# Performance work log

Measured on AMD Instinct MI355X. Metric: run time of the kernel, lower is better.

Reference implementation:

```python
import jax, jax.numpy as jnp
import numpy as np

B, S, H, E, K = 4, 4096, 2048, 64, 8
SEQ_ALPHA = 0.01


def setup_inputs() -> dict:
    key = jax.random.key(0)
    k1, k2 = jax.random.split(key)
    x = jax.random.normal(k1, (B, S, H), dtype=jnp.float32)
    # kaiming_uniform_(a=sqrt(5)) on [E, H] -> bound = 1/sqrt(H)
    bound = 1.0 / np.sqrt(H)
    weight = jax.random.uniform(k2, (E, H), dtype=jnp.float32, minval=-bound, maxval=bound)
    expert_bias = jnp.zeros((E,), dtype=jnp.float32)
    return {"x": x, "weight": weight, "expert_bias": expert_bias}


def reference(x, weight, expert_bias):
    bsz, seq_len, _ = x.shape
    x_flat = x.reshape(-1, x.shape[-1])                      # [T, H], T = B*S
    logits = x_flat @ weight.T                               # [T, E]
    scores = jax.nn.sigmoid(logits)
    biased_logits = logits + expert_bias[None, :]
    _, topk_idx = jax.lax.top_k(biased_logits, K)            # [T, K] int32
    topk_w = jnp.take_along_axis(scores, topk_idx, axis=-1)  # [T, K]
    topk_w = topk_w / (topk_w.sum(axis=-1, keepdims=True) + 1e-10)  # K > 1
    # load stats (training-mode bincount)
    expert_load = jnp.bincount(topk_idx.reshape(-1), length=E).astype(jnp.int64)
    # sequence-wise balance loss (DeepSeek-V3)
    scores_r = scores.reshape(bsz, seq_len, E)
    expert_mask = jax.nn.one_hot(topk_idx.reshape(bsz, -1), E, dtype=scores.dtype)  # [B, S*K, E]
    f_i = expert_mask.sum(axis=1) / (K * seq_len)            # [B, E]
    normalized = scores_r / (scores_r.sum(axis=2, keepdims=True) + 1e-10)
    P_i = normalized.mean(axis=1)                            # [B, E]
    aux_seq_loss = SEQ_ALPHA * (f_i * P_i).sum(axis=1).mean()
    return (topk_idx, topk_w, aux_seq_loss, expert_load)
```

## Files before the change

kernel.cpp:

```cpp
#include <hip/hip_runtime.h>
#include <math.h>

#define HDIM 2048
#define TTOK 16384
#define NEXP 64
#define TOPK 8
#define SLEN 4096
#define NBATCH 4

#define OFF_W    131072
#define OFF_LOSS 262144
#define OFF_LOAD 262145

#define WS_PACC 0
#define WS_CACC 256
#define WS_CNT  512
#define WS_WH   1024
#define WS_WL   (1024 + 65536)

using s16x8 = __attribute__((ext_vector_type(8))) short;
using f32x4 = __attribute__((ext_vector_type(4))) float;

__device__ __forceinline__ unsigned bfh(float v) {
  unsigned b = __float_as_uint(v);
  return (b + 0x7FFFu + ((b >> 16) & 1u)) >> 16;
}

__device__ __forceinline__ void split4(float4 v, uint2* hi, uint2* lo) {
  unsigned h0 = bfh(v.x), h1 = bfh(v.y), h2 = bfh(v.z), h3 = bfh(v.w);
  float r0 = v.x - __uint_as_float(h0 << 16);
  float r1 = v.y - __uint_as_float(h1 << 16);
  float r2 = v.z - __uint_as_float(h2 << 16);
  float r3 = v.w - __uint_as_float(h3 << 16);
  unsigned l0 = bfh(r0), l1 = bfh(r1), l2 = bfh(r2), l3 = bfh(r3);
  *hi = make_uint2(h0 | (h1 << 16), h2 | (h3 << 16));
  *lo = make_uint2(l0 | (l1 << 16), l2 | (l3 << 16));
}

__global__ __launch_bounds__(256) void prep_w(const float* __restrict__ W,
                                              ushort* __restrict__ Wh,
                                              ushort* __restrict__ Wl) {
  const int i = (blockIdx.x * 256 + threadIdx.x) << 2;
  float4 v = *(const float4*)(W + i);
  uint2 hp, lp;
  split4(v, &hp, &lp);
  *(uint2*)(Wh + i) = hp;
  *(uint2*)(Wl + i) = lp;
}

__global__ __launch_bounds__(1024) void gate_fused(
    const float* __restrict__ x,
    const ushort* __restrict__ Whg,
    const ushort* __restrict__ Wlg,
    const float* __restrict__ bias,
    float* __restrict__ out, float* __restrict__ Pacc,
    float* __restrict__ Cacc, int* __restrict__ counter) {
  __shared__ ushort XhL[2][4096];
  __shared__ ushort XlL[2][4096];
  __shared__ ushort WhL[2][4096];
  __shared__ ushort WlL[2][4096];
  __shared__ float le[64 * 65];
  __shared__ float sgm[64 * 65];
  __shared__ float rinvs[64];
  __shared__ float biasl[64];
  __shared__ unsigned csum[64];
  __shared__ int lastf;

  const int tid = threadIdx.x;
  const int lane = tid & 63;
  const int wv = __builtin_amdgcn_readfirstlane(tid >> 6);
  const int tok0 = blockIdx.x << 6;

  if (tid < 64) { csum[tid] = 0u; biasl[tid] = bias[tid]; }

  const int srow = tid >> 4;
  const int skq = (tid & 15) << 2;
  const int sdst = (srow << 6) + (((skq >> 3) ^ (srow & 7)) << 3) +
                   (((skq >> 2) & 1) << 2);
  const float* xsrc = x + (size_t)(tok0 + srow) * HDIM + skq;
  const ushort* whsrc = Whg + ((size_t)srow << 11) + skq;
  const ushort* wlsrc = Wlg + ((size_t)srow << 11) + skq;

  float4 xA = *(const float4*)xsrc;
  float4 xB = *(const float4*)(xsrc + 64);
  uint2 whA = *(const uint2*)whsrc;
  uint2 whB = *(const uint2*)(whsrc + 64);
  uint2 wlA = *(const uint2*)wlsrc;
  uint2 wlB = *(const uint2*)(wlsrc + 64);

  const int mt = wv >> 2, nt = wv & 3;
  const int fl = lane & 15, fg = lane >> 4;
  const int arow = (mt << 4) + fl;
  const int brow = (nt << 4) + fl;
  const int ab0 = (arow << 6) + ((fg ^ (arow & 7)) << 3);
  const int ab1 = (arow << 6) + (((fg + 4) ^ (arow & 7)) << 3);
  const int bb0 = (brow << 6) + ((fg ^ (brow & 7)) << 3);
  const int bb1 = (brow << 6) + (((fg + 4) ^ (brow & 7)) << 3);

  f32x4 acc = {0.f, 0.f, 0.f, 0.f};

  constexpr int NT = HDIM / 64;
  for (int kt = 0; kt < NT; ++kt) {
    const int cur = kt & 1;
    {
      uint2 hp, lp;
      split4(xA, &hp, &lp);
      *(uint2*)&XhL[cur][sdst] = hp;
      *(uint2*)&XlL[cur][sdst] = lp;
      *(uint2*)&WhL[cur][sdst] = whA;
      *(uint2*)&WlL[cur][sdst] = wlA;
    }
    __syncthreads();
    xA = xB; whA = whB; wlA = wlB;
    if (kt + 2 < NT) {
      xB = *(const float4*)(xsrc + ((kt + 2) << 6));
      whB = *(const uint2*)(whsrc + ((kt + 2) << 6));
      wlB = *(const uint2*)(wlsrc + ((kt + 2) << 6));
    }
    s16x8 ah0 = *(const s16x8*)&XhL[cur][ab0];
    s16x8 al0 = *(const s16x8*)&XlL[cur][ab0];
    s16x8 bh0 = *(const s16x8*)&WhL[cur][bb0];
    s16x8 bl0 = *(const s16x8*)&WlL[cur][bb0];
    acc = __builtin_amdgcn_mfma_f32_16x16x32_bf16(al0, bh0, acc, 0, 0, 0);
    acc = __builtin_amdgcn_mfma_f32_16x16x32_bf16(ah0, bl0, acc, 0, 0, 0);
    acc = __builtin_amdgcn_mfma_f32_16x16x32_bf16(ah0, bh0, acc, 0, 0, 0);
    s16x8 ah1 = *(const s16x8*)&XhL[cur][ab1];
    s16x8 al1 = *(const s16x8*)&XlL[cur][ab1];
    s16x8 bh1 = *(const s16x8*)&WhL[cur][bb1];
    s16x8 bl1 = *(const s16x8*)&WlL[cur][bb1];
    acc = __builtin_amdgcn_mfma_f32_16x16x32_bf16(al1, bh1, acc, 0, 0, 0);
    acc = __builtin_amdgcn_mfma_f32_16x16x32_bf16(ah1, bl1, acc, 0, 0, 0);
    acc = __builtin_amdgcn_mfma_f32_16x16x32_bf16(ah1, bh1, acc, 0, 0, 0);
  }

  {
    const int trow = (mt << 4) + (fg << 2);
    const int ecol = (nt << 4) + fl;
#pragma unroll
    for (int r = 0; r < 4; ++r) {
      float lg = acc[r];
      le[(trow + r) * 65 + ecol] = lg;
      sgm[(trow + r) * 65 + ecol] = 1.f / (1.f + expf(-lg));
    }
  }
  __syncthreads();

  const int b = (int)(blockIdx.x >> 6);

  if (wv == 0) {
    const int t = lane;
    float bl[64];
#pragma unroll
    for (int e = 0; e < NEXP; ++e) bl[e] = le[t * 65 + e] + biasl[e];

    unsigned long long chosen = 0ull;
    int i8[TOPK];
    float w8[TOPK];
    float wsum = 0.f;
#pragma unroll
    for (int j = 0; j < TOPK; ++j) {
      float best = -1e30f;
      int bi = 0;
#pragma unroll
      for (int e = 0; e < NEXP; ++e) {
        bool ok = (((chosen >> e) & 1ull) == 0ull) && (bl[e] > best);
        if (ok) { best = bl[e]; bi = e; }
      }
      chosen |= (1ull << bi);
      float sc = sgm[t * 65 + bi];
      i8[j] = bi;
      w8[j] = sc;
      wsum += sc;
    }
    const float inv = 1.f / (wsum + 1e-10f);
    const int tt = tok0 + t;
    float4 o;
    o.x = (float)i8[0]; o.y = (float)i8[1]; o.z = (float)i8[2]; o.w = (float)i8[3];
    *(float4*)(out + (size_t)tt * TOPK) = o;
    o.x = (float)i8[4]; o.y = (float)i8[5]; o.z = (float)i8[6]; o.w = (float)i8[7];
    *(float4*)(out + (size_t)tt * TOPK + 4) = o;
    o.x = w8[0] * inv; o.y = w8[1] * inv; o.z = w8[2] * inv; o.w = w8[3] * inv;
    *(float4*)(out + OFF_W + (size_t)tt * TOPK) = o;
    o.x = w8[4] * inv; o.y = w8[5] * inv; o.z = w8[6] * inv; o.w = w8[7] * inv;
    *(float4*)(out + OFF_W + (size_t)tt * TOPK + 4) = o;
#pragma unroll
    for (int j = 0; j < TOPK; ++j) atomicAdd(&csum[i8[j]], 1u);
    atomicAdd(&Cacc[(b << 6) + lane], (float)csum[lane]);
  } else if (wv == 1) {
    const int t = lane;
    float ss = 0.f;
    for (int e = 0; e < NEXP; ++e) ss += sgm[t * 65 + e];
    rinvs[t] = 1.f / (ss + 1e-10f);
    float p = 0.f;
    for (int t2 = 0; t2 < 64; ++t2) p += sgm[t2 * 65 + lane] * rinvs[t2];
    atomicAdd(&Pacc[(b << 6) + lane], p);
  }

  __syncthreads();
  __threadfence();
  if (tid == 0) {
    int old = __hip_atomic_fetch_add(counter, 1, __ATOMIC_ACQ_REL,
                                     __HIP_MEMORY_SCOPE_AGENT);
    lastf = (old == 255) ? 1 : 0;
  }
  __syncthreads();

  if (lastf && tid < 64) {
    const int e = tid;
    float load = 0.f, partl = 0.f;
#pragma unroll
    for (int bb = 0; bb < NBATCH; ++bb) {
      float c = __hip_atomic_load(&Cacc[(bb << 6) + e], __ATOMIC_RELAXED,
                                  __HIP_MEMORY_SCOPE_AGENT);
      float p = __hip_atomic_load(&Pacc[(bb << 6) + e], __ATOMIC_RELAXED,
                                  __HIP_MEMORY_SCOPE_AGENT);
      load += c;
      partl += (c * (1.f / (TOPK * (float)SLEN))) * (p * (1.f / (float)SLEN));
    }
    out[OFF_LOAD + e] = load;
#pragma unroll
    for (int off = 32; off; off >>= 1) partl += __shfl_down(partl, off);
    if (e == 0) out[OFF_LOSS] = 0.01f * partl * (1.f / (float)NBATCH);
  }
}

extern "C" void kernel_launch(void* const* d_in, const int* in_sizes, int n_in,
                              void* d_out, int out_size, void* d_ws, size_t ws_size,
                              hipStream_t stream) {
  const float* x = (const float*)d_in[0];
  const float* W = (const float*)d_in[1];
  const float* bias = (const float*)d_in[2];
  float* out = (float*)d_out;

  float* ws = (float*)d_ws;
  float* Pacc = ws + WS_PACC;
  float* Cacc = ws + WS_CACC;
  int* counter = (int*)(ws + WS_CNT);
  ushort* Wh = (ushort*)(ws + WS_WH);
  ushort* Wl = (ushort*)(ws + WS_WL);

  hipMemsetAsync(ws, 0, 1024 * sizeof(float), stream);
  prep_w<<<128, 256, 0, stream>>>(W, Wh, Wl);
  gate_fused<<<256, 1024, 0, stream>>>(x, Wh, Wl, bias, out, Pacc, Cacc, counter);
}
```

Baseline: 287.0 us.

## Use 16-token tiles with weights pre-swizzled into MFMA fragment layout read from global

Repacks the split bf16 weight into a per-lane MFMA fragment layout so each wave loads its B operands straight from global/L2 instead of staging them through LDS. Blocks shrink from 64 tokens and 1024 threads to 16 tokens and 256 threads, giving 1024 blocks and much less shared memory per block so more blocks fit per CU. The trade-off is that the weight is re-read from cache by four times as many blocks, and the top-k stage now uses only 16 lanes of one wave.

```diff
diff --git a/kernel.cpp b/kernel.cpp
--- a/kernel.cpp
+++ b/kernel.cpp
@@ -15,8 +15,9 @@
 #define WS_PACC 0
 #define WS_CACC 256
 #define WS_CNT  512
-#define WS_WH   1024
-#define WS_WL   (1024 + 65536)
+#define WS_WF   1024
+#define WFLO    131072
+#define NBLK    1024
 
 using s16x8 = __attribute__((ext_vector_type(8))) short;
 using f32x4 = __attribute__((ext_vector_type(4))) float;
@@ -37,39 +38,50 @@
   *lo = make_uint2(l0 | (l1 << 16), l2 | (l3 << 16));
 }
 
-__global__ __launch_bounds__(256) void prep_w(const float* __restrict__ W,
-                                              ushort* __restrict__ Wh,
-                                              ushort* __restrict__ Wl) {
-  const int i = (blockIdx.x * 256 + threadIdx.x) << 2;
-  float4 v = *(const float4*)(W + i);
-  uint2 hp, lp;
-  split4(v, &hp, &lp);
-  *(uint2*)(Wh + i) = hp;
-  *(uint2*)(Wl + i) = lp;
-}
-
-__global__ __launch_bounds__(1024) void gate_fused(
+__global__ __launch_bounds__(256) void prep_wf(const float* __restrict__ W,
+                                               ushort* __restrict__ WF) {
+  const int id = blockIdx.x * 256 + threadIdx.x;
+  const int lane = id & 63;
+  const int reg = (id >> 6) & 1;
+  const int nt = (id >> 7) & 3;
+  const int kt = (id >> 9) & 31;
+  const int plane = id >> 14;
+  const int e = (nt << 4) + (lane & 15);
+  const int k0 = (kt << 6) + (reg << 5) + ((lane >> 4) << 3);
+  const float* src = W + (size_t)e * HDIM + k0;
+  unsigned w[4];
+#pragma unroll
+  for (int j = 0; j < 4; ++j) {
+    float v0 = src[2 * j], v1 = src[2 * j + 1];
+    unsigned h0 = bfh(v0), h1 = bfh(v1);
+    if (plane) {
+      h0 = bfh(v0 - __uint_as_float(h0 << 16));
+      h1 = bfh(v1 - __uint_as_float(h1 << 16));
+    }
+    w[j] = h0 | (h1 << 16);
+  }
+  *(uint4*)(WF + ((size_t)id << 3)) = make_uint4(w[0], w[1], w[2], w[3]);
+}
+
+__global__ __launch_bounds__(256, 8) void gate_fused(
     const float* __restrict__ x,
-    const ushort* __restrict__ Whg,
-    const ushort* __restrict__ Wlg,
+    const ushort* __restrict__ WF,
     const float* __restrict__ bias,
     float* __restrict__ out, float* __restrict__ Pacc,
     float* __restrict__ Cacc, int* __restrict__ counter) {
-  __shared__ ushort XhL[2][4096];
-  __shared__ ushort XlL[2][4096];
-  __shared__ ushort WhL[2][4096];
-  __shared__ ushort WlL[2][4096];
-  __shared__ float le[64 * 65];
-  __shared__ float sgm[64 * 65];
-  __shared__ float rinvs[64];
+  __shared__ ushort XhL[2][1024];
+  __shared__ ushort XlL[2][1024];
+  __shared__ float le[16 * 65];
+  __shared__ float sgm[16 * 65];
+  __shared__ float rinvs[16];
   __shared__ float biasl[64];
   __shared__ unsigned csum[64];
   __shared__ int lastf;
 
   const int tid = threadIdx.x;
   const int lane = tid & 63;
-  const int wv = __builtin_amdgcn_readfirstlane(tid >> 6);
-  const int tok0 = blockIdx.x << 6;
+  const int nt = __builtin_amdgcn_readfirstlane(tid >> 6);
+  const int tok0 = blockIdx.x << 4;
 
   if (tid < 64) { csum[tid] = 0u; biasl[tid] = bias[tid]; }
 
@@ -78,24 +90,14 @@
   const int sdst = (srow << 6) + (((skq >> 3) ^ (srow & 7)) << 3) +
                    (((skq >> 2) & 1) << 2);
   const float* xsrc = x + (size_t)(tok0 + srow) * HDIM + skq;
-  const ushort* whsrc = Whg + ((size_t)srow << 11) + skq;
-  const ushort* wlsrc = Wlg + ((size_t)srow << 11) + skq;
-
   float4 xA = *(const float4*)xsrc;
   float4 xB = *(const float4*)(xsrc + 64);
-  uint2 whA = *(const uint2*)whsrc;
-  uint2 whB = *(const uint2*)(whsrc + 64);
-  uint2 wlA = *(const uint2*)wlsrc;
-  uint2 wlB = *(const uint2*)(wlsrc + 64);
-
-  const int mt = wv >> 2, nt = wv & 3;
+
   const int fl = lane & 15, fg = lane >> 4;
-  const int arow = (mt << 4) + fl;
-  const int brow = (nt << 4) + fl;
+  const int arow = fl;
   const int ab0 = (arow << 6) + ((fg ^ (arow & 7)) << 3);
   const int ab1 = (arow << 6) + (((fg + 4) ^ (arow & 7)) << 3);
-  const int bb0 = (brow << 6) + ((fg ^ (brow & 7)) << 3);
-  const int bb1 = (brow << 6) + (((fg + 4) ^ (brow & 7)) << 3);
+  const ushort* wbase = WF + ((size_t)((nt << 7) + lane) << 3);
 
   f32x4 acc = {0.f, 0.f, 0.f, 0.f};
 
@@ -107,34 +109,29 @@
       split4(xA, &hp, &lp);
       *(uint2*)&XhL[cur][sdst] = hp;
       *(uint2*)&XlL[cur][sdst] = lp;
-      *(uint2*)&WhL[cur][sdst] = whA;
-      *(uint2*)&WlL[cur][sdst] = wlA;
     }
     __syncthreads();
-    xA = xB; whA = whB; wlA = wlB;
-    if (kt + 2 < NT) {
-      xB = *(const float4*)(xsrc + ((kt + 2) << 6));
-      whB = *(const uint2*)(whsrc + ((kt + 2) << 6));
-      wlB = *(const uint2*)(wlsrc + ((kt + 2) << 6));
-    }
+    xA = xB;
+    if (kt + 2 < NT) xB = *(const float4*)(xsrc + ((kt + 2) << 6));
+    const ushort* whp = wbase + (kt << 12);
+    s16x8 bh0 = *(const s16x8*)whp;
+    s16x8 bh1 = *(const s16x8*)(whp + 512);
+    s16x8 bl0 = *(const s16x8*)(whp + WFLO);
+    s16x8 bl1 = *(const s16x8*)(whp + WFLO + 512);
     s16x8 ah0 = *(const s16x8*)&XhL[cur][ab0];
     s16x8 al0 = *(const s16x8*)&XlL[cur][ab0];
-    s16x8 bh0 = *(const s16x8*)&WhL[cur][bb0];
-    s16x8 bl0 = *(const s16x8*)&WlL[cur][bb0];
+    s16x8 ah1 = *(const s16x8*)&XhL[cur][ab1];
+    s16x8 al1 = *(const s16x8*)&XlL[cur][ab1];
     acc = __builtin_amdgcn_mfma_f32_16x16x32_bf16(al0, bh0, acc, 0, 0, 0);
     acc = __builtin_amdgcn_mfma_f32_16x16x32_bf16(ah0, bl0, acc, 0, 0, 0);
     acc = __builtin_amdgcn_mfma_f32_16x16x32_bf16(ah0, bh0, acc, 0, 0, 0);
-    s16x8 ah1 = *(const s16x8*)&XhL[cur][ab1];
-    s16x8 al1 = *(const s16x8*)&XlL[cur][ab1];
-    s16x8 bh1 = *(const s16x8*)&WhL[cur][bb1];
-    s16x8 bl1 = *(const s16x8*)&WlL[cur][bb1];
     acc = __builtin_amdgcn_mfma_f32_16x16x32_bf16(al1, bh1, acc, 0, 0, 0);
     acc = __builtin_amdgcn_mfma_f32_16x16x32_bf16(ah1, bl1, acc, 0, 0, 0);
     acc = __builtin_amdgcn_mfma_f32_16x16x32_bf16(ah1, bh1, acc, 0, 0, 0);
   }
 
   {
-    const int trow = (mt << 4) + (fg << 2);
+    const int trow = fg << 2;
     const int ecol = (nt << 4) + fl;
 #pragma unroll
     for (int r = 0; r < 4; ++r) {
@@ -145,54 +142,59 @@
   }
   __syncthreads();
 
-  const int b = (int)(blockIdx.x >> 6);
-
-  if (wv == 0) {
-    const int t = lane;
-    float bl[64];
-#pragma unroll
-    for (int e = 0; e < NEXP; ++e) bl[e] = le[t * 65 + e] + biasl[e];
-
-    unsigned long long chosen = 0ull;
-    int i8[TOPK];
-    float w8[TOPK];
-    float wsum = 0.f;
-#pragma unroll
-    for (int j = 0; j < TOPK; ++j) {
-      float best = -1e30f;
-      int bi = 0;
-#pragma unroll
-      for (int e = 0; e < NEXP; ++e) {
-        bool ok = (((chosen >> e) & 1ull) == 0ull) && (bl[e] > best);
-        if (ok) { best = bl[e]; bi = e; }
+  const int b = (int)(blockIdx.x >> 8);
+
+  if (nt == 0) {
+    if (lane < 16) {
+      const int t = lane;
+      float bl[64];
+#pragma unroll
+      for (int e = 0; e < NEXP; ++e) bl[e] = le[t * 65 + e] + biasl[e];
+
+      unsigned long long chosen = 0ull;
+      int i8[TOPK];
+      float w8[TOPK];
+      float wsum = 0.f;
+#pragma unroll
+      for (int j = 0; j < TOPK; ++j) {
+        float best = -1e30f;
+        int bi = 0;
+#pragma unroll
+        for (int e = 0; e < NEXP; ++e) {
+          bool ok = (((chosen >> e) & 1ull) == 0ull) && (bl[e] > best);
+          if (ok) { best = bl[e]; bi = e; }
+        }
+        chosen |= (1ull << bi);
+        float sc = sgm[t * 65 + bi];
+        i8[j] = bi;
+        w8[j] = sc;
+        wsum += sc;
       }
-      chosen |= (1ull << bi);
-      float sc = sgm[t * 65 + bi];
-      i8[j] = bi;
-      w8[j] = sc;
-      wsum += sc;
-    }
-    const float inv = 1.f / (wsum + 1e-10f);
-    const int tt = tok0 + t;
-    float4 o;
-    o.x = (float)i8[0]; o.y = (float)i8[1]; o.z = (float)i8[2]; o.w = (float)i8[3];
-    *(float4*)(out + (size_t)tt * TOPK) = o;
-    o.x = (float)i8[4]; o.y = (float)i8[5]; o.z = (float)i8[6]; o.w = (float)i8[7];
-    *(float4*)(out + (size_t)tt * TOPK + 4) = o;
-    o.x = w8[0] * inv; o.y = w8[1] * inv; o.z = w8[2] * inv; o.w = w8[3] * inv;
-    *(float4*)(out + OFF_W + (size_t)tt * TOPK) = o;
-    o.x = w8[4] * inv; o.y = w8[5] * inv; o.z = w8[6] * inv; o.w = w8[7] * inv;
-    *(float4*)(out + OFF_W + (size_t)tt * TOPK + 4) = o;
-#pragma unroll
-    for (int j = 0; j < TOPK; ++j) atomicAdd(&csum[i8[j]], 1u);
+      const float inv = 1.f / (wsum + 1e-10f);
+      const int tt = tok0 + t;
+      float4 o;
+      o.x = (float)i8[0]; o.y = (float)i8[1]; o.z = (float)i8[2]; o.w = (float)i8[3];
+      *(float4*)(out + (size_t)tt * TOPK) = o;
+      o.x = (float)i8[4]; o.y = (float)i8[5]; o.z = (float)i8[6]; o.w = (float)i8[7];
+      *(float4*)(out + (size_t)tt * TOPK + 4) = o;
+      o.x = w8[0] * inv; o.y = w8[1] * inv; o.z = w8[2] * inv; o.w = w8[3] * inv;
+      *(float4*)(out + OFF_W + (size_t)tt * TOPK) = o;
+      o.x = w8[4] * inv; o.y = w8[5] * inv; o.z = w8[6] * inv; o.w = w8[7] * inv;
+      *(float4*)(out + OFF_W + (size_t)tt * TOPK + 4) = o;
+#pragma unroll
+      for (int j = 0; j < TOPK; ++j) atomicAdd(&csum[i8[j]], 1u);
+    }
     atomicAdd(&Cacc[(b << 6) + lane], (float)csum[lane]);
-  } else if (wv == 1) {
-    const int t = lane;
-    float ss = 0.f;
-    for (int e = 0; e < NEXP; ++e) ss += sgm[t * 65 + e];
-    rinvs[t] = 1.f / (ss + 1e-10f);
+  } else if (nt == 1) {
+    if (lane < 16) {
+      const int t = lane;
+      float ss = 0.f;
+      for (int e = 0; e < NEXP; ++e) ss += sgm[t * 65 + e];
+      rinvs[t] = 1.f / (ss + 1e-10f);
+    }
     float p = 0.f;
-    for (int t2 = 0; t2 < 64; ++t2) p += sgm[t2 * 65 + lane] * rinvs[t2];
+#pragma unroll
+    for (int t2 = 0; t2 < 16; ++t2) p += sgm[t2 * 65 + lane] * rinvs[t2];
     atomicAdd(&Pacc[(b << 6) + lane], p);
   }
 
@@ -201,7 +203,7 @@
   if (tid == 0) {
     int old = __hip_atomic_fetch_add(counter, 1, __ATOMIC_ACQ_REL,
                                      __HIP_MEMORY_SCOPE_AGENT);
-    lastf = (old == 255) ? 1 : 0;
+    lastf = (old == NBLK - 1) ? 1 : 0;
   }
   __syncthreads();
 
@@ -236,10 +238,9 @@
   float* Pacc = ws + WS_PACC;
   float* Cacc = ws + WS_CACC;
   int* counter = (int*)(ws + WS_CNT);
-  ushort* Wh = (ushort*)(ws + WS_WH);
-  ushort* Wl = (ushort*)(ws + WS_WL);
+  ushort* WF = (ushort*)(ws + WS_WF);
 
   hipMemsetAsync(ws, 0, 1024 * sizeof(float), stream);
-  prep_w<<<128, 256, 0, stream>>>(W, Wh, Wl);
-  gate_fused<<<256, 1024, 0, stream>>>(x, Wh, Wl, bias, out, Pacc, Cacc, counter);
-}
+  prep_wf<<<128, 256, 0, stream>>>(W, WF);
+  gate_fused<<<NBLK, 256, 0, stream>>>(x, WF, bias, out, Pacc, Cacc, counter);
+}
```

Result: slower. 321.7 us (+12.1%).
